# Optimization experiments

Hardware: AMD Instinct MI355X
Metric: run time of the kernel (lower is better)

Reference implementation:

```python
import jax, jax.numpy as jnp
import numpy as np

EPS = 1e-5
NEG_SLOPE = 0.01  # F.leaky_relu default

N0, N1, N2 = 100000, 25000, 5000
E0, E1 = 800000, 160000
D_IN, D_HID, D_OUT = 256, 256, 128


def setup_inputs() -> dict:
    key = jax.random.key(0)
    ks = jax.random.split(key, 16)
    inp = {
        "x": jax.random.normal(ks[0], (N0, D_IN), dtype=jnp.float32),
        "src0": jax.random.randint(ks[1], (E0,), 0, N0, dtype=jnp.int32),
        "dst0": jax.random.randint(ks[2], (E0,), 0, N1, dtype=jnp.int32),
        "val0": jnp.arange(E0, dtype=jnp.int32),
        "src1": jax.random.randint(ks[3], (E1,), 0, N1, dtype=jnp.int32),
        "dst1": jax.random.randint(ks[4], (E1,), 0, N2, dtype=jnp.int32),
        "val1": jnp.arange(E1, dtype=jnp.int32),
        "timestamps": jax.random.randint(ks[5], (E0 + E1,), 0, 100, dtype=jnp.int32),
        "time": 50,
        "interval": 10,
        # SAGEConv layer 1 (in -> hidden): lin_l (bias) on aggregated, lin_r (no bias) on root
        "W1l": jax.random.normal(ks[6], (D_IN, D_HID), dtype=jnp.float32) / np.sqrt(D_IN),
        "W1r": jax.random.normal(ks[7], (D_IN, D_HID), dtype=jnp.float32) / np.sqrt(D_IN),
        "b1": jnp.zeros((D_HID,), dtype=jnp.float32),
        # BatchNorm1d params (eval mode: running stats)
        "g1": jnp.ones((D_HID,), dtype=jnp.float32),
        "bt1": jnp.zeros((D_HID,), dtype=jnp.float32),
        "rm1": jax.random.normal(ks[8], (D_HID,), dtype=jnp.float32) * 0.1,
        "rv1": jax.random.uniform(ks[9], (D_HID,), dtype=jnp.float32) + 0.5,
        # SAGEConv layer 2 (hidden -> out)
        "W2l": jax.random.normal(ks[10], (D_HID, D_OUT), dtype=jnp.float32) / np.sqrt(D_HID),
        "W2r": jax.random.normal(ks[11], (D_HID, D_OUT), dtype=jnp.float32) / np.sqrt(D_HID),
        "b2": jnp.zeros((D_OUT,), dtype=jnp.float32),
    }
    return inp


def _time_mask(val, timestamps, time, interval):
    # time_sparse keeps edges whose timestamp is in {time, ..., time+interval-1}
    ts = timestamps[val]
    return (ts >= time) & (ts < time + interval)


def _sage_conv(x_src, x_tgt, src, dst, mask, Wl, Wr, b, n_tgt):
    m = mask.astype(x_src.dtype)
    msg = x_src[src] * m[:, None]               # [E, D] gather + mask
    agg = jax.ops.segment_sum(msg, dst, num_segments=n_tgt)
    deg = jax.ops.segment_sum(m, dst, num_segments=n_tgt)
    agg = agg / jnp.maximum(deg, 1.0)[:, None]  # mean aggregation
    return agg @ Wl + b + x_tgt @ Wr


def reference(x, src0, dst0, val0, src1, dst1, val1, timestamps, time, interval,
              W1l, W1r, b1, g1, bt1, rm1, rv1, W2l, W2r, b2):
    # layer 0: N0 -> N1
    mask0 = _time_mask(val0, timestamps, time, interval)
    h = _sage_conv(x, x[:N1], src0, dst0, mask0, W1l, W1r, b1, N1)
    # BatchNorm1d (eval) + leaky_relu; dropout is identity in eval
    h = (h - rm1) * jax.lax.rsqrt(rv1 + EPS) * g1 + bt1
    h = jnp.where(h >= 0, h, NEG_SLOPE * h)
    # layer 1: N1 -> N2
    mask1 = _time_mask(val1, timestamps, time, interval)
    out = _sage_conv(h, h[:N2], src1, dst1, mask1, W2l, W2r, b2, N2)
    return out, mask1
```

## Files before the change

### kernel.cpp

```cpp
#include <hip/hip_runtime.h>

#define N1c 25000
#define N2c 5000
#define Dc 256
#define DOUTc 128
#define EPSc 1e-5f
#define NEGc 0.01f

typedef __attribute__((ext_vector_type(8))) short short8;
typedef __attribute__((ext_vector_type(4))) float f32x4;

__device__ __forceinline__ ushort f2bf(float f) {
    unsigned u = __float_as_uint(f);
    u += 0x7fffu + ((u >> 16) & 1u);
    return (ushort)(u >> 16);
}
__device__ __forceinline__ float bf2f(ushort u) {
    return __uint_as_float(((unsigned)u) << 16);
}
__device__ __forceinline__ unsigned pack2(float lo, float hi) {
    return ((unsigned)f2bf(lo)) | (((unsigned)f2bf(hi)) << 16);
}

__global__ __launch_bounds__(256) void prep_all(
    const int* __restrict__ dst0, const int* __restrict__ val0,
    const int* __restrict__ dst1, const int* __restrict__ val1,
    const int* __restrict__ ts, const int* __restrict__ time_p, const int* __restrict__ itv_p,
    const float* __restrict__ W1l, const float* __restrict__ W1r,
    const float* __restrict__ W2l, const float* __restrict__ W2r,
    int E0, int E1,
    ushort* __restrict__ Bt1, ushort* __restrict__ Bt2,
    int* __restrict__ count0, int* __restrict__ count1,
    float* __restrict__ mask_out) {
    const int flat = blockIdx.x * blockDim.x + threadIdx.x;
    const int NT = gridDim.x * blockDim.x;
    const int t0 = *time_p, iv = *itv_p;

    for (int i = flat; i < 256 * 512; i += NT) {
        int n = i >> 9, k = i & 511;
        float v = (k < 256) ? W1l[(size_t)k * 256 + n] : W1r[(size_t)(k - 256) * 256 + n];
        Bt1[i] = f2bf(v);
    }
    for (int i = flat; i < 128 * 512; i += NT) {
        int n = i >> 9, k = i & 511;
        float v = (k < 256) ? W2l[(size_t)k * 128 + n] : W2r[(size_t)(k - 256) * 128 + n];
        Bt2[i] = f2bf(v);
    }
    for (int e = flat; e < E1; e += NT) {
        int t = ts[val1[e]];
        mask_out[e] = (t >= t0 && t < t0 + iv) ? 1.0f : 0.0f;
    }
    for (int e = flat; e < E0; e += NT) {
        int t = ts[val0[e]];
        if (t >= t0 && t < t0 + iv) atomicAdd(&count0[dst0[e]], 1);
    }
    for (int e = flat; e < E1; e += NT) {
        int t = ts[val1[e]];
        if (t >= t0 && t < t0 + iv) atomicAdd(&count1[dst1[e]], 1);
    }
}

template <int CH>
__device__ __forceinline__ void scan_block(const int* __restrict__ count,
                                           int* __restrict__ offsets, int n) {
    __shared__ int wsum[16];
    int t = threadIdx.x;
    int lane = t & 63, w = t >> 6;
    int v[CH];
    int base = t * CH;
    int run = 0;
#pragma unroll
    for (int i = 0; i < CH; ++i) {
        int c = (base + i < n) ? count[base + i] : 0;
        v[i] = run;
        run += c;
    }
    int incl = run;
#pragma unroll
    for (int off = 1; off < 64; off <<= 1) {
        int s = __shfl_up(incl, off, 64);
        if (lane >= off) incl += s;
    }
    if (lane == 63) wsum[w] = incl;
    __syncthreads();
    if (t == 0) {
        int s = 0;
#pragma unroll
        for (int i = 0; i < 16; ++i) { int c = wsum[i]; wsum[i] = s; s += c; }
    }
    __syncthreads();
    int pre = wsum[w] + (incl - run);
#pragma unroll
    for (int i = 0; i < CH; ++i) {
        int idx = base + i;
        if (idx < n) offsets[idx] = pre + v[i];
    }
}

__global__ __launch_bounds__(1024) void scan_both(
    const int* __restrict__ count0, int* __restrict__ offsets0,
    const int* __restrict__ count1, int* __restrict__ offsets1) {
    if (blockIdx.x == 0) scan_block<25>(count0, offsets0, N1c);
    else                 scan_block<5>(count1, offsets1, N2c);
}

__global__ __launch_bounds__(256) void fill_both(
    const int* __restrict__ src0, const int* __restrict__ dst0, const int* __restrict__ val0,
    const int* __restrict__ src1, const int* __restrict__ dst1, const int* __restrict__ val1,
    const int* __restrict__ ts, const int* __restrict__ time_p, const int* __restrict__ itv_p,
    int E0, int E1,
    int* __restrict__ offsets0, int* __restrict__ offsets1,
    int* __restrict__ eidx0, int* __restrict__ eidx1) {
    int e = blockIdx.x * blockDim.x + threadIdx.x;
    int t0 = *time_p, iv = *itv_p;
    if (e < E0) {
        int t = ts[val0[e]];
        if (t >= t0 && t < t0 + iv) {
            int pos = atomicAdd(&offsets0[dst0[e]], 1);
            eidx0[pos] = src0[e];
        }
    } else if (e < E0 + E1) {
        int e1 = e - E0;
        int t = ts[val1[e1]];
        if (t >= t0 && t < t0 + iv) {
            int pos = atomicAdd(&offsets1[dst1[e1]], 1);
            eidx1[pos] = src1[e1];
        }
    }
}

__global__ void gather_f32(const float* __restrict__ X,
                           const int* __restrict__ off,
                           const int* __restrict__ eidx,
                           ushort* __restrict__ agg, int n) {
    int wave = (blockIdx.x * blockDim.x + threadIdx.x) >> 6;
    int lane = threadIdx.x & 63;
    if (wave >= n) return;
    int s1 = off[wave];
    int s0 = wave ? off[wave - 1] : 0;
    float4 acc = make_float4(0.f, 0.f, 0.f, 0.f);
    for (int j = s0; j < s1; ++j) {
        int s = eidx[j];
        float4 v = *(const float4*)(X + (size_t)s * Dc + lane * 4);
        acc.x += v.x; acc.y += v.y; acc.z += v.z; acc.w += v.w;
    }
    float inv = 1.0f / fmaxf((float)(s1 - s0), 1.0f);
    ushort4 o;
    o.x = f2bf(acc.x * inv); o.y = f2bf(acc.y * inv);
    o.z = f2bf(acc.z * inv); o.w = f2bf(acc.w * inv);
    *(ushort4*)(agg + (size_t)wave * Dc + lane * 4) = o;
}

__global__ void gather_bf16(const ushort* __restrict__ H,
                            const int* __restrict__ off,
                            const int* __restrict__ eidx,
                            ushort* __restrict__ agg, int n) {
    int wave = (blockIdx.x * blockDim.x + threadIdx.x) >> 6;
    int lane = threadIdx.x & 63;
    if (wave >= n) return;
    int s1 = off[wave];
    int s0 = wave ? off[wave - 1] : 0;
    float4 acc = make_float4(0.f, 0.f, 0.f, 0.f);
    for (int j = s0; j < s1; ++j) {
        int s = eidx[j];
        ushort4 v = *(const ushort4*)(H + (size_t)s * Dc + lane * 4);
        acc.x += bf2f(v.x); acc.y += bf2f(v.y);
        acc.z += bf2f(v.z); acc.w += bf2f(v.w);
    }
    float inv = 1.0f / fmaxf((float)(s1 - s0), 1.0f);
    ushort4 o;
    o.x = f2bf(acc.x * inv); o.y = f2bf(acc.y * inv);
    o.z = f2bf(acc.z * inv); o.w = f2bf(acc.w * inv);
    *(ushort4*)(agg + (size_t)wave * Dc + lane * 4) = o;
}

template <int VARIANT, int GRPS>
__global__ __launch_bounds__(128) void gemm_mfma(
    const ushort* __restrict__ Alo,
    const ushort* __restrict__ A2b, const float* __restrict__ A2f,
    const ushort* __restrict__ Bt,
    const float* __restrict__ bias,
    const float* __restrict__ g, const float* __restrict__ bt,
    const float* __restrict__ rm, const float* __restrict__ rv,
    void* __restrict__ Cout, int M) {
    constexpr int BM = 32 * GRPS;
    constexpr int TPR = 128 / BM;
    constexpr int CHUNK = 32 / TPR;
    __shared__ ushort As[BM][40];
    __shared__ ushort Bs[128][40];
    int tid = threadIdx.x;
    int wave = tid >> 6, lane = tid & 63;
    int quad = lane >> 4, l16 = lane & 15;
    int m0 = blockIdx.y * BM, n0 = blockIdx.x * 128;
    f32x4 acc[GRPS][8] = {};
    int ar = tid / TPR;
    int ak = (tid % TPR) * CHUNK;
    int bn = tid;
    for (int k0 = 0; k0 < 512; k0 += 32) {
        uint4 a0 = make_uint4(0, 0, 0, 0), a1 = make_uint4(0, 0, 0, 0);
        bool inb = (m0 + ar) < M;
        if (k0 < 256) {
            if (inb) {
                const ushort* Ag = Alo + (size_t)(m0 + ar) * Dc + k0 + ak;
                a0 = *(const uint4*)Ag;
                if (CHUNK == 16) a1 = *(const uint4*)(Ag + 8);
            }
        } else if (VARIANT == 0) {
            if (inb) {
                const float* Af = A2f + (size_t)(m0 + ar) * Dc + (k0 - 256) + ak;
                float4 f0 = *(const float4*)(Af + 0);
                float4 f1 = *(const float4*)(Af + 4);
                a0 = make_uint4(pack2(f0.x, f0.y), pack2(f0.z, f0.w),
                                pack2(f1.x, f1.y), pack2(f1.z, f1.w));
                if (CHUNK == 16) {
                    float4 f2 = *(const float4*)(Af + 8);
                    float4 f3 = *(const float4*)(Af + 12);
                    a1 = make_uint4(pack2(f2.x, f2.y), pack2(f2.z, f2.w),
                                    pack2(f3.x, f3.y), pack2(f3.z, f3.w));
                }
            }
        } else {
            if (inb) {
                const ushort* Ag = A2b + (size_t)(m0 + ar) * Dc + (k0 - 256) + ak;
                a0 = *(const uint4*)Ag;
                if (CHUNK == 16) a1 = *(const uint4*)(Ag + 8);
            }
        }
        const ushort* Bg = Bt + (size_t)(n0 + bn) * 512 + k0;
        uint4 b0 = *(const uint4*)(Bg + 0);
        uint4 b1 = *(const uint4*)(Bg + 8);
        uint4 b2 = *(const uint4*)(Bg + 16);
        uint4 b3 = *(const uint4*)(Bg + 24);
        __syncthreads();
        *(uint4*)&As[ar][ak] = a0;
        if (CHUNK == 16) *(uint4*)&As[ar][ak + 8] = a1;
        *(uint4*)&Bs[bn][0] = b0;
        *(uint4*)&Bs[bn][8] = b1;
        *(uint4*)&Bs[bn][16] = b2;
        *(uint4*)&Bs[bn][24] = b3;
        __syncthreads();
        short8 af[GRPS];
#pragma unroll
        for (int grp = 0; grp < GRPS; ++grp)
            af[grp] = *(const short8*)&As[wave * 16 * GRPS + grp * 16 + l16][quad * 8];
#pragma unroll
        for (int j = 0; j < 8; ++j) {
            short8 bf = *(const short8*)&Bs[j * 16 + l16][quad * 8];
#pragma unroll
            for (int grp = 0; grp < GRPS; ++grp)
                acc[grp][j] = __builtin_amdgcn_mfma_f32_16x16x32_bf16(af[grp], bf, acc[grp][j], 0, 0, 0);
        }
    }
#pragma unroll
    for (int grp = 0; grp < GRPS; ++grp) {
#pragma unroll
        for (int j = 0; j < 8; ++j) {
            int gn = n0 + j * 16 + l16;
            float sc = 1.f, sh = bias[gn];
            if (VARIANT == 0) {
                float s = g[gn] * rsqrtf(rv[gn] + EPSc);
                sh = (bias[gn] - rm[gn]) * s + bt[gn];
                sc = s;
            }
            int gmb = m0 + wave * 16 * GRPS + grp * 16 + quad * 4;
#pragma unroll
            for (int r = 0; r < 4; ++r) {
                int gm = gmb + r;
                if (gm >= M) continue;
                float v = acc[grp][j][r];
                if (VARIANT == 0) {
                    v = v * sc + sh;
                    v = v >= 0.f ? v : NEGc * v;
                    ((ushort*)Cout)[(size_t)gm * Dc + gn] = f2bf(v);
                } else {
                    ((float*)Cout)[(size_t)gm * DOUTc + gn] = v + sh;
                }
            }
        }
    }
}

extern "C" void kernel_launch(void* const* d_in, const int* in_sizes, int n_in,
                              void* d_out, int out_size, void* d_ws, size_t ws_size,
                              hipStream_t stream) {
    const float* x    = (const float*)d_in[0];
    const int* src0   = (const int*)d_in[1];
    const int* dst0   = (const int*)d_in[2];
    const int* val0   = (const int*)d_in[3];
    const int* src1   = (const int*)d_in[4];
    const int* dst1   = (const int*)d_in[5];
    const int* val1   = (const int*)d_in[6];
    const int* ts     = (const int*)d_in[7];
    const int* time_p = (const int*)d_in[8];
    const int* itv_p  = (const int*)d_in[9];
    const float* W1l  = (const float*)d_in[10];
    const float* W1r  = (const float*)d_in[11];
    const float* b1   = (const float*)d_in[12];
    const float* g1   = (const float*)d_in[13];
    const float* bt1  = (const float*)d_in[14];
    const float* rm1  = (const float*)d_in[15];
    const float* rv1  = (const float*)d_in[16];
    const float* W2l  = (const float*)d_in[17];
    const float* W2r  = (const float*)d_in[18];
    const float* b2   = (const float*)d_in[19];
    int E0 = in_sizes[1];
    int E1 = in_sizes[4];
    float* out = (float*)d_out;

    ushort* agg0 = (ushort*)d_ws;
    ushort* h    = agg0 + (size_t)N1c * Dc;
    ushort* agg1 = h    + (size_t)N1c * Dc;
    ushort* Bt1  = agg1 + (size_t)N2c * Dc;
    ushort* Bt2  = Bt1  + 256 * 512;
    int* ip      = (int*)(Bt2 + 128 * 512);
    int* count0   = ip;            ip += N1c;
    int* count1   = ip;            ip += N2c;
    int* offsets0 = ip;            ip += N1c;
    int* offsets1 = ip;            ip += N2c;
    int* eidx0    = ip;            ip += E0;
    int* eidx1    = ip;            ip += E1;
    float* mask_tail = out + (size_t)N2c * DOUTc;

    hipMemsetAsync(count0, 0, (size_t)(N1c + N2c) * sizeof(int), stream);

    prep_all<<<1024, 256, 0, stream>>>(
        dst0, val0, dst1, val1, ts, time_p, itv_p,
        W1l, W1r, W2l, W2r, E0, E1, Bt1, Bt2, count0, count1, mask_tail);
    scan_both<<<2, 1024, 0, stream>>>(count0, offsets0, count1, offsets1);
    fill_both<<<(E0 + E1 + 255) / 256, 256, 0, stream>>>(
        src0, dst0, val0, src1, dst1, val1, ts, time_p, itv_p,
        E0, E1, offsets0, offsets1, eidx0, eidx1);
    gather_f32<<<(N1c + 3) / 4, 256, 0, stream>>>(x, offsets0, eidx0, agg0, N1c);
    gemm_mfma<0, 2><<<dim3(2, (N1c + 63) / 64), 128, 0, stream>>>(
        agg0, nullptr, x, Bt1, b1, g1, bt1, rm1, rv1, h, N1c);
    gather_bf16<<<(N2c + 3) / 4, 256, 0, stream>>>(h, offsets1, eidx1, agg1, N2c);
    gemm_mfma<1, 1><<<dim3(1, (N2c + 31) / 32), 128, 0, stream>>>(
        agg1, h, nullptr, Bt2, b2, nullptr, nullptr, nullptr, nullptr, out, N2c);
}
```

Before: 278.9 us.

## Fuse neighbor mean-aggregation gathers into the SAGE GEMM kernels via shared memory

The separate gather kernels are removed. Each GEMM block now computes the mean-aggregated neighbor rows for its own M tile directly into LDS, then runs the MFMA loop over them. This avoids writing and re-reading the bf16 agg0/agg1 buffers and saves two kernel launches. The layer-0 GEMM now covers all 256 output columns in one block with 256 threads and 64 rows. This raises LDS use and accumulator register pressure, and the serial gather phase cannot overlap with MFMA work inside a block.

```diff
diff --git a/kernel.cpp b/kernel.cpp
--- a/kernel.cpp
+++ b/kernel.cpp
@@ -129,153 +129,169 @@
     }
 }
 
-__global__ void gather_f32(const float* __restrict__ X,
-                           const int* __restrict__ off,
-                           const int* __restrict__ eidx,
-                           ushort* __restrict__ agg, int n) {
-    int wave = (blockIdx.x * blockDim.x + threadIdx.x) >> 6;
-    int lane = threadIdx.x & 63;
-    if (wave >= n) return;
-    int s1 = off[wave];
-    int s0 = wave ? off[wave - 1] : 0;
-    float4 acc = make_float4(0.f, 0.f, 0.f, 0.f);
-    for (int j = s0; j < s1; ++j) {
-        int s = eidx[j];
-        float4 v = *(const float4*)(X + (size_t)s * Dc + lane * 4);
-        acc.x += v.x; acc.y += v.y; acc.z += v.z; acc.w += v.w;
-    }
-    float inv = 1.0f / fmaxf((float)(s1 - s0), 1.0f);
-    ushort4 o;
-    o.x = f2bf(acc.x * inv); o.y = f2bf(acc.y * inv);
-    o.z = f2bf(acc.z * inv); o.w = f2bf(acc.w * inv);
-    *(ushort4*)(agg + (size_t)wave * Dc + lane * 4) = o;
-}
-
-__global__ void gather_bf16(const ushort* __restrict__ H,
-                            const int* __restrict__ off,
-                            const int* __restrict__ eidx,
-                            ushort* __restrict__ agg, int n) {
-    int wave = (blockIdx.x * blockDim.x + threadIdx.x) >> 6;
-    int lane = threadIdx.x & 63;
-    if (wave >= n) return;
-    int s1 = off[wave];
-    int s0 = wave ? off[wave - 1] : 0;
-    float4 acc = make_float4(0.f, 0.f, 0.f, 0.f);
-    for (int j = s0; j < s1; ++j) {
-        int s = eidx[j];
-        ushort4 v = *(const ushort4*)(H + (size_t)s * Dc + lane * 4);
-        acc.x += bf2f(v.x); acc.y += bf2f(v.y);
-        acc.z += bf2f(v.z); acc.w += bf2f(v.w);
-    }
-    float inv = 1.0f / fmaxf((float)(s1 - s0), 1.0f);
-    ushort4 o;
-    o.x = f2bf(acc.x * inv); o.y = f2bf(acc.y * inv);
-    o.z = f2bf(acc.z * inv); o.w = f2bf(acc.w * inv);
-    *(ushort4*)(agg + (size_t)wave * Dc + lane * 4) = o;
-}
-
-template <int VARIANT, int GRPS>
-__global__ __launch_bounds__(128) void gemm_mfma(
-    const ushort* __restrict__ Alo,
-    const ushort* __restrict__ A2b, const float* __restrict__ A2f,
+__global__ __launch_bounds__(256) void gemm0_fused(
+    const float* __restrict__ x,
+    const int* __restrict__ off, const int* __restrict__ eidx,
     const ushort* __restrict__ Bt,
     const float* __restrict__ bias,
     const float* __restrict__ g, const float* __restrict__ bt,
     const float* __restrict__ rm, const float* __restrict__ rv,
-    void* __restrict__ Cout, int M) {
-    constexpr int BM = 32 * GRPS;
-    constexpr int TPR = 128 / BM;
-    constexpr int CHUNK = 32 / TPR;
-    __shared__ ushort As[BM][40];
+    ushort* __restrict__ h, int M) {
+    __shared__ ushort Af[64][264];
+    __shared__ ushort As2[64][40];
+    __shared__ ushort Bs[256][40];
+    int tid = threadIdx.x;
+    int wave = tid >> 6, lane = tid & 63;
+    int quad = lane >> 4, l16 = lane & 15;
+    int m0 = blockIdx.x * 64;
+
+    for (int i = wave; i < 64; i += 4) {
+        int row = m0 + i;
+        float4 acc = make_float4(0.f, 0.f, 0.f, 0.f);
+        int deg = 0;
+        if (row < M) {
+            int s1 = off[row], s0 = row ? off[row - 1] : 0;
+            deg = s1 - s0;
+            for (int j = s0; j < s1; ++j) {
+                int s = eidx[j];
+                float4 v = *(const float4*)(x + (size_t)s * Dc + lane * 4);
+                acc.x += v.x; acc.y += v.y; acc.z += v.z; acc.w += v.w;
+            }
+        }
+        float inv = 1.0f / fmaxf((float)deg, 1.0f);
+        ushort4 o;
+        o.x = f2bf(acc.x * inv); o.y = f2bf(acc.y * inv);
+        o.z = f2bf(acc.z * inv); o.w = f2bf(acc.w * inv);
+        *(ushort4*)&Af[i][lane * 4] = o;
+    }
+    __syncthreads();
+
+    f32x4 acc[16] = {};
+    int bn = tid;
+    int ar2 = tid >> 2;
+    int ak2 = (tid & 3) * 8;
+    for (int k0 = 0; k0 < 512; k0 += 32) {
+        const ushort* Bg = Bt + (size_t)bn * 512 + k0;
+        uint4 b0 = *(const uint4*)(Bg + 0);
+        uint4 b1 = *(const uint4*)(Bg + 8);
+        uint4 b2 = *(const uint4*)(Bg + 16);
+        uint4 b3 = *(const uint4*)(Bg + 24);
+        uint4 a2 = make_uint4(0, 0, 0, 0);
+        if (k0 >= 256 && m0 + ar2 < M) {
+            const float* Ap = x + (size_t)(m0 + ar2) * Dc + (k0 - 256) + ak2;
+            float4 f0 = *(const float4*)(Ap + 0);
+            float4 f1 = *(const float4*)(Ap + 4);
+            a2 = make_uint4(pack2(f0.x, f0.y), pack2(f0.z, f0.w),
+                            pack2(f1.x, f1.y), pack2(f1.z, f1.w));
+        }
+        __syncthreads();
+        *(uint4*)&Bs[bn][0]  = b0;
+        *(uint4*)&Bs[bn][8]  = b1;
+        *(uint4*)&Bs[bn][16] = b2;
+        *(uint4*)&Bs[bn][24] = b3;
+        if (k0 >= 256) *(uint4*)&As2[ar2][ak2] = a2;
+        __syncthreads();
+        short8 af = (k0 < 256)
+            ? *(const short8*)&Af[wave * 16 + l16][k0 + quad * 8]
+            : *(const short8*)&As2[wave * 16 + l16][quad * 8];
+#pragma unroll
+        for (int j = 0; j < 16; ++j) {
+            short8 bf = *(const short8*)&Bs[j * 16 + l16][quad * 8];
+            acc[j] = __builtin_amdgcn_mfma_f32_16x16x32_bf16(af, bf, acc[j], 0, 0, 0);
+        }
+    }
+#pragma unroll
+    for (int j = 0; j < 16; ++j) {
+        int gn = j * 16 + l16;
+        float s = g[gn] * rsqrtf(rv[gn] + EPSc);
+        float sh = (bias[gn] - rm[gn]) * s + bt[gn];
+        int gmb = m0 + wave * 16 + quad * 4;
+#pragma unroll
+        for (int r = 0; r < 4; ++r) {
+            int gm = gmb + r;
+            if (gm >= M) continue;
+            float v = acc[j][r] * s + sh;
+            v = v >= 0.f ? v : NEGc * v;
+            h[(size_t)gm * Dc + gn] = f2bf(v);
+        }
+    }
+}
+
+__global__ __launch_bounds__(128) void gemm1_fused(
+    const ushort* __restrict__ hsrc,
+    const int* __restrict__ off, const int* __restrict__ eidx,
+    const ushort* __restrict__ Bt,
+    const float* __restrict__ bias,
+    float* __restrict__ out, int M) {
+    __shared__ ushort Af[32][264];
+    __shared__ ushort As2[32][40];
     __shared__ ushort Bs[128][40];
     int tid = threadIdx.x;
     int wave = tid >> 6, lane = tid & 63;
     int quad = lane >> 4, l16 = lane & 15;
-    int m0 = blockIdx.y * BM, n0 = blockIdx.x * 128;
-    f32x4 acc[GRPS][8] = {};
-    int ar = tid / TPR;
-    int ak = (tid % TPR) * CHUNK;
+    int m0 = blockIdx.x * 32;
+
+    for (int i = wave; i < 32; i += 2) {
+        int row = m0 + i;
+        float4 acc = make_float4(0.f, 0.f, 0.f, 0.f);
+        int deg = 0;
+        if (row < M) {
+            int s1 = off[row], s0 = row ? off[row - 1] : 0;
+            deg = s1 - s0;
+            for (int j = s0; j < s1; ++j) {
+                int s = eidx[j];
+                ushort4 v = *(const ushort4*)(hsrc + (size_t)s * Dc + lane * 4);
+                acc.x += bf2f(v.x); acc.y += bf2f(v.y);
+                acc.z += bf2f(v.z); acc.w += bf2f(v.w);
+            }
+        }
+        float inv = 1.0f / fmaxf((float)deg, 1.0f);
+        ushort4 o;
+        o.x = f2bf(acc.x * inv); o.y = f2bf(acc.y * inv);
+        o.z = f2bf(acc.z * inv); o.w = f2bf(acc.w * inv);
+        *(ushort4*)&Af[i][lane * 4] = o;
+    }
+    __syncthreads();
+
+    f32x4 acc[8] = {};
     int bn = tid;
+    int ar2 = tid >> 2;
+    int ak2 = (tid & 3) * 8;
     for (int k0 = 0; k0 < 512; k0 += 32) {
-        uint4 a0 = make_uint4(0, 0, 0, 0), a1 = make_uint4(0, 0, 0, 0);
-        bool inb = (m0 + ar) < M;
-        if (k0 < 256) {
-            if (inb) {
-                const ushort* Ag = Alo + (size_t)(m0 + ar) * Dc + k0 + ak;
-                a0 = *(const uint4*)Ag;
-                if (CHUNK == 16) a1 = *(const uint4*)(Ag + 8);
-            }
-        } else if (VARIANT == 0) {
-            if (inb) {
-                const float* Af = A2f + (size_t)(m0 + ar) * Dc + (k0 - 256) + ak;
-                float4 f0 = *(const float4*)(Af + 0);
-                float4 f1 = *(const float4*)(Af + 4);
-                a0 = make_uint4(pack2(f0.x, f0.y), pack2(f0.z, f0.w),
-                                pack2(f1.x, f1.y), pack2(f1.z, f1.w));
-                if (CHUNK == 16) {
-                    float4 f2 = *(const float4*)(Af + 8);
-                    float4 f3 = *(const float4*)(Af + 12);
-                    a1 = make_uint4(pack2(f2.x, f2.y), pack2(f2.z, f2.w),
-                                    pack2(f3.x, f3.y), pack2(f3.z, f3.w));
-                }
-            }
-        } else {
-            if (inb) {
-                const ushort* Ag = A2b + (size_t)(m0 + ar) * Dc + (k0 - 256) + ak;
-                a0 = *(const uint4*)Ag;
-                if (CHUNK == 16) a1 = *(const uint4*)(Ag + 8);
-            }
-        }
-        const ushort* Bg = Bt + (size_t)(n0 + bn) * 512 + k0;
+        const ushort* Bg = Bt + (size_t)bn * 512 + k0;
         uint4 b0 = *(const uint4*)(Bg + 0);
         uint4 b1 = *(const uint4*)(Bg + 8);
         uint4 b2 = *(const uint4*)(Bg + 16);
         uint4 b3 = *(const uint4*)(Bg + 24);
+        uint4 a2 = make_uint4(0, 0, 0, 0);
+        if (k0 >= 256 && m0 + ar2 < M)
+            a2 = *(const uint4*)(hsrc + (size_t)(m0 + ar2) * Dc + (k0 - 256) + ak2);
         __syncthreads();
-        *(uint4*)&As[ar][ak] = a0;
-        if (CHUNK == 16) *(uint4*)&As[ar][ak + 8] = a1;
-        *(uint4*)&Bs[bn][0] = b0;
-        *(uint4*)&Bs[bn][8] = b1;
+        *(uint4*)&Bs[bn][0]  = b0;
+        *(uint4*)&Bs[bn][8]  = b1;
         *(uint4*)&Bs[bn][16] = b2;
         *(uint4*)&Bs[bn][24] = b3;
+        if (k0 >= 256) *(uint4*)&As2[ar2][ak2] = a2;
         __syncthreads();
-        short8 af[GRPS];
-#pragma unroll
-        for (int grp = 0; grp < GRPS; ++grp)
-            af[grp] = *(const short8*)&As[wave * 16 * GRPS + grp * 16 + l16][quad * 8];
+        short8 af = (k0 < 256)
+            ? *(const short8*)&Af[wave * 16 + l16][k0 + quad * 8]
+            : *(const short8*)&As2[wave * 16 + l16][quad * 8];
 #pragma unroll
         for (int j = 0; j < 8; ++j) {
             short8 bf = *(const short8*)&Bs[j * 16 + l16][quad * 8];
-#pragma unroll
-            for (int grp = 0; grp < GRPS; ++grp)
-                acc[grp][j] = __builtin_amdgcn_mfma_f32_16x16x32_bf16(af[grp], bf, acc[grp][j], 0, 0, 0);
-        }
-    }
-#pragma unroll
-    for (int grp = 0; grp < GRPS; ++grp) {
-#pragma unroll
-        for (int j = 0; j < 8; ++j) {
-            int gn = n0 + j * 16 + l16;
-            float sc = 1.f, sh = bias[gn];
-            if (VARIANT == 0) {
-                float s = g[gn] * rsqrtf(rv[gn] + EPSc);
-                sh = (bias[gn] - rm[gn]) * s + bt[gn];
-                sc = s;
-            }
-            int gmb = m0 + wave * 16 * GRPS + grp * 16 + quad * 4;
-#pragma unroll
-            for (int r = 0; r < 4; ++r) {
-                int gm = gmb + r;
-                if (gm >= M) continue;
-                float v = acc[grp][j][r];
-                if (VARIANT == 0) {
-                    v = v * sc + sh;
-                    v = v >= 0.f ? v : NEGc * v;
-                    ((ushort*)Cout)[(size_t)gm * Dc + gn] = f2bf(v);
-                } else {
-                    ((float*)Cout)[(size_t)gm * DOUTc + gn] = v + sh;
-                }
-            }
+            acc[j] = __builtin_amdgcn_mfma_f32_16x16x32_bf16(af, bf, acc[j], 0, 0, 0);
+        }
+    }
+#pragma unroll
+    for (int j = 0; j < 8; ++j) {
+        int gn = j * 16 + l16;
+        float sh = bias[gn];
+        int gmb = m0 + wave * 16 + quad * 4;
+#pragma unroll
+        for (int r = 0; r < 4; ++r) {
+            int gm = gmb + r;
+            if (gm >= M) continue;
+            out[(size_t)gm * DOUTc + gn] = acc[j][r] + sh;
         }
     }
 }
@@ -307,11 +323,9 @@
     int E1 = in_sizes[4];
     float* out = (float*)d_out;
 
-    ushort* agg0 = (ushort*)d_ws;
-    ushort* h    = agg0 + (size_t)N1c * Dc;
-    ushort* agg1 = h    + (size_t)N1c * Dc;
-    ushort* Bt1  = agg1 + (size_t)N2c * Dc;
-    ushort* Bt2  = Bt1  + 256 * 512;
+    ushort* h    = (ushort*)d_ws;
+    ushort* Bt1  = h + (size_t)N1c * Dc;
+    ushort* Bt2  = Bt1 + 256 * 512;
     int* ip      = (int*)(Bt2 + 128 * 512);
     int* count0   = ip;            ip += N1c;
     int* count1   = ip;            ip += N2c;
@@ -330,10 +344,8 @@
     fill_both<<<(E0 + E1 + 255) / 256, 256, 0, stream>>>(
         src0, dst0, val0, src1, dst1, val1, ts, time_p, itv_p,
         E0, E1, offsets0, offsets1, eidx0, eidx1);
-    gather_f32<<<(N1c + 3) / 4, 256, 0, stream>>>(x, offsets0, eidx0, agg0, N1c);
-    gemm_mfma<0, 2><<<dim3(2, (N1c + 63) / 64), 128, 0, stream>>>(
-        agg0, nullptr, x, Bt1, b1, g1, bt1, rm1, rv1, h, N1c);
-    gather_bf16<<<(N2c + 3) / 4, 256, 0, stream>>>(h, offsets1, eidx1, agg1, N2c);
-    gemm_mfma<1, 1><<<dim3(1, (N2c + 31) / 32), 128, 0, stream>>>(
-        agg1, h, nullptr, Bt2, b2, nullptr, nullptr, nullptr, nullptr, out, N2c);
-}
+    gemm0_fused<<<(N1c + 63) / 64, 256, 0, stream>>>(
+        x, offsets0, eidx0, Bt1, b1, g1, bt1, rm1, rv1, h, N1c);
+    gemm1_fused<<<(N2c + 31) / 32, 128, 0, stream>>>(
+        h, offsets1, eidx1, Bt2, b2, out, N2c);
+}
```

New measurement: 332.2 us. +19.1%, slower.
